# Optimization experiments

Measured on AMD Instinct MI355X. Metric: run time of the kernel, lower is better.

The kernel has to match this reference:

```python
import jax, jax.numpy as jnp
import numpy as np

E = 1024  # embed_dim
H = 16    # num_heads
D = E // H  # head_dim


def setup_inputs() -> dict:
    key = jax.random.key(0)
    ks = jax.random.split(key, 9)
    s = 0.02
    return {
        "hidden_state": jax.random.normal(ks[0], (4, 1024, E), jnp.float32),
        "Wq": jax.random.normal(ks[1], (H, D, E), jnp.float32) * s,
        "bq": jax.random.normal(ks[2], (H, D), jnp.float32) * s,
        "Wk": jax.random.normal(ks[3], (H, D, E), jnp.float32) * s,
        "bk": jax.random.normal(ks[4], (H, D), jnp.float32) * s,
        "Wv": jax.random.normal(ks[5], (H, D, E), jnp.float32) * s,
        "bv": jax.random.normal(ks[6], (H, D), jnp.float32) * s,
        "Wo": jax.random.normal(ks[7], (E, E), jnp.float32) * s,
        "bo": jax.random.normal(ks[8], (E,), jnp.float32) * s,
    }


def _mha(x, Wq, bq, Wk, bk, Wv, bv, Wo, bo):
    # Per-head linear projections (torch Linear: y = x W^T + b), batched over heads.
    q = jnp.einsum("bse,hde->bhsd", x, Wq) + bq[None, :, None, :]
    k = jnp.einsum("bse,hde->bhsd", x, Wk) + bk[None, :, None, :]
    v = jnp.einsum("bse,hde->bhsd", x, Wv) + bv[None, :, None, :]
    scores = jnp.einsum("bhsd,bhtd->bhst", q, k) / jnp.sqrt(jnp.asarray(D, x.dtype))
    w = jax.nn.softmax(scores, axis=-1)  # F.softmax default -> last dim
    o = jnp.einsum("bhst,bhtd->bhsd", w, v)
    # concat heads along last dim: [B,S,H*D] in head order (matches torch.cat)
    B, _, S, _ = o.shape
    o = jnp.transpose(o, (0, 2, 1, 3)).reshape(B, S, H * D)
    return o @ Wo.T + bo


def reference(hidden_state, Wq, bq, Wk, bk, Wv, bv, Wo, bo):
    return _mha(hidden_state, Wq, bq, Wk, bk, Wv, bv, Wo, bo)
```

## Files before the change

### kernel.cpp

```cpp
#include <hip/hip_runtime.h>
#include <hip/hip_bf16.h>
#include <stdint.h>

#define E_DIM 1024
#define H_NUM 16
#define D_DIM 64
#define B_NUM 4
#define S_LEN 1024

typedef __attribute__((ext_vector_type(8))) short bf16x8;
typedef __attribute__((ext_vector_type(4))) short bf16x4;
typedef __attribute__((ext_vector_type(4))) float f32x4;

#define SOFTMAX_C2 0.18033688011112042f

__device__ inline ushort f2b(float x) {
    __hip_bfloat16 h = __float2bfloat16(x);
    return *(ushort*)&h;
}
__device__ inline float b2f(ushort u) {
    __hip_bfloat16 h = *(__hip_bfloat16*)&u;
    return __bfloat162float(h);
}
__device__ inline uint pk2(float a, float b) {
    __hip_bfloat162 h = __float22bfloat162_rn(make_float2(a, b));
    return *(uint*)&h;
}
__device__ inline float fexp2(float x) { return __builtin_amdgcn_exp2f(x); }

__device__ inline uint pk2h(float a, float b) {
    uint ua = __builtin_bit_cast(uint, a) + 0x8000u;
    uint ub = __builtin_bit_cast(uint, b) + 0x8000u;
    return __builtin_amdgcn_perm(ub, ua, 0x07060302u);
}

__device__ inline void gld16(const ushort* g, ushort* l) {
    __builtin_amdgcn_global_load_lds((const __attribute__((address_space(1))) void*)g,
                                     (__attribute__((address_space(3))) void*)l, 16, 0, 0);
}

__global__ __launch_bounds__(256)
void convert_all(const float* __restrict__ X,  const float* __restrict__ Wq,
                 const float* __restrict__ Wk, const float* __restrict__ Wv,
                 const float* __restrict__ Wo,
                 ushort* __restrict__ Xb, ushort* __restrict__ Wcat,
                 ushort* __restrict__ Wob)
{
    const int bid = blockIdx.x;
    const float* src; ushort* dst; size_t off;
    if (bid < 4096)      { src = X;  dst = Xb;   off = (size_t)bid * 1024; }
    else if (bid < 5120) { src = Wq; dst = Wcat;              off = (size_t)(bid - 4096) * 1024; }
    else if (bid < 6144) { src = Wk; dst = Wcat + (1u << 20); off = (size_t)(bid - 5120) * 1024; }
    else if (bid < 7168) { src = Wv; dst = Wcat + (2u << 20); off = (size_t)(bid - 6144) * 1024; }
    else                 { src = Wo; dst = Wob;               off = (size_t)(bid - 7168) * 1024; }
    const size_t i = off + (size_t)threadIdx.x * 4;
    float4 v = *(const float4*)&src[i];
    ushort4 o;
    o.x = f2b(v.x); o.y = f2b(v.y); o.z = f2b(v.z); o.w = f2b(v.w);
    *(ushort4*)&dst[i] = o;
}

__global__ __launch_bounds__(256, 4)
void gemm_qkv(const ushort* __restrict__ A, const ushort* __restrict__ Bw,
              const float* __restrict__ b0, const float* __restrict__ b1,
              const float* __restrict__ b2,
              ushort* __restrict__ Qb, ushort* __restrict__ Kb,
              ushort* __restrict__ Vt_g, int K)
{
    __shared__ __align__(16) ushort SM[17408];
    ushort* As = SM;
    ushort* Bs = SM + 8192;

    const int tid  = threadIdx.x;
    const int wave = tid >> 6;
    const int lane = tid & 63;
    const int quad = lane >> 4;
    const int l16  = lane & 15;
    const int wm   = wave & 1;
    const int wn   = wave >> 1;

    const int bid = blockIdx.x;
    const int xcd = bid & 7;
    const int j   = bid >> 3;
    const int jm  = j / 24;
    const int jn  = j - jm * 24;
    const int m0  = (xcd * 4 + jm) * 128;
    const int n0  = jn * 128;

    f32x4 acc[4][4] = {};

    auto stageA = [&](int k0) {
#pragma unroll
        for (int i = 0; i < 4; ++i) {
            const int e   = i * 256 + tid;
            const int row = e >> 3;
            const int gc8 = ((e & 7) ^ (row & 7)) * 8;
            gld16(&A[(size_t)(m0 + row) * K + k0 + gc8], &As[e * 8]);
        }
    };
    auto stageB = [&](int k0) {
#pragma unroll
        for (int i = 0; i < 4; ++i) {
            const int e   = i * 256 + tid;
            const int row = e >> 3;
            const int gc8 = ((e & 7) ^ (row & 7)) * 8;
            gld16(&Bw[(size_t)(n0 + row) * K + k0 + gc8], &Bs[e * 8]);
        }
    };

    const int nk = K >> 6;
    const int xa = (l16 & 7) * 8;
    for (int ki = 0; ki < nk; ++ki) {
        stageA(ki << 6); stageB(ki << 6);
        __syncthreads();

#pragma unroll
        for (int ks = 0; ks < 2; ++ks) {
            const int lc = (ks * 32 + quad * 8) ^ xa;
            bf16x8 af[4], bf[4];
#pragma unroll
            for (int mi = 0; mi < 4; ++mi)
                af[mi] = *(const bf16x8*)&As[(wm * 64 + mi * 16 + l16) * 64 + lc];
#pragma unroll
            for (int ni = 0; ni < 4; ++ni)
                bf[ni] = *(const bf16x8*)&Bs[(wn * 64 + ni * 16 + l16) * 64 + lc];
#pragma unroll
            for (int mi = 0; mi < 4; ++mi)
#pragma unroll
                for (int ni = 0; ni < 4; ++ni)
                    acc[mi][ni] = __builtin_amdgcn_mfma_f32_16x16x32_bf16(af[mi], bf[ni], acc[mi][ni], 0, 0, 0);
        }
        __syncthreads();
    }

    const int seg   = n0 >> 10;
    const int cbase = n0 & 1023;
    const float* bp = (seg == 0) ? b0 : (seg == 1) ? b1 : b2;
    const float scl = (seg == 0) ? SOFTMAX_C2 : 1.0f;

    if (seg < 2) {
        ushort* T = SM;
#pragma unroll
        for (int ni = 0; ni < 4; ++ni) {
            const int nloc = wn * 64 + ni * 16 + l16;
            const float bv = bp[cbase + nloc];
#pragma unroll
            for (int mi = 0; mi < 4; ++mi)
#pragma unroll
                for (int r = 0; r < 4; ++r)
                    T[(wm * 64 + mi * 16 + quad * 4 + r) * 136 + nloc] =
                        f2b((acc[mi][ni][r] + bv) * scl);
        }
        __syncthreads();
        ushort* dst = (seg == 0) ? Qb : Kb;
        const int row = tid >> 1, half = tid & 1;
        const ushort* s = &T[row * 136 + half * 64];
        ushort* d = &dst[(size_t)(m0 + row) * 1024 + cbase + half * 64];
#pragma unroll
        for (int j2 = 0; j2 < 8; ++j2)
            *(uint4*)(d + j2 * 8) = *(const uint4*)(s + j2 * 8);
    } else {
        ushort* Tt = SM;
        const int b  = m0 >> 10, sbase = m0 & 1023;
#pragma unroll
        for (int ni = 0; ni < 4; ++ni) {
            const int nloc = wn * 64 + ni * 16 + l16;
            const float bv = bp[cbase + nloc];
#pragma unroll
            for (int mi = 0; mi < 4; ++mi) {
                const int mloc = wm * 64 + mi * 16 + quad * 4;
                ushort4 pk;
                pk.x = f2b(acc[mi][ni][0] + bv);
                pk.y = f2b(acc[mi][ni][1] + bv);
                pk.z = f2b(acc[mi][ni][2] + bv);
                pk.w = f2b(acc[mi][ni][3] + bv);
                *(ushort4*)&Tt[nloc * 136 + mloc] = pk;
            }
        }
        __syncthreads();
        const int nrow = tid >> 1, half = tid & 1;
        const int hh   = (cbase >> 6) + (nrow >> 6);
        const int drow = nrow & 63;
        const ushort* s = &Tt[nrow * 136 + half * 64];
        ushort* d = &Vt_g[(((size_t)(b * 16 + hh)) * 64 + drow) * 1024 + sbase + half * 64];
#pragma unroll
        for (int j2 = 0; j2 < 8; ++j2)
            *(uint4*)(d + j2 * 8) = *(const uint4*)(s + j2 * 8);
    }
}

__global__ __launch_bounds__(256, 4)
void attention16(const ushort* __restrict__ Qg, const ushort* __restrict__ Kg,
                 const ushort* __restrict__ Vg, ushort* __restrict__ Anorm)
{
    __shared__ __align__(16) ushort SM[16896];
    const int VOFF = 8192;

    const int tid  = threadIdx.x;
    const int w    = tid >> 6;
    const int lane = tid & 63;
    const int quad = lane >> 4;
    const int l16  = lane & 15;

    const int gid = blockIdx.x;
    const int qt  = (gid >> 3) & 15;
    const int bh  = (gid & 7) | ((gid >> 7) << 3);
    const int b   = bh >> 4;
    const int h   = bh & 15;
    const size_t tbase = ((size_t)b * S_LEN) * E_DIM + (size_t)h * D_DIM;
    const size_t vbase = (size_t)bh * D_DIM * S_LEN;

    const ushort* qrow = Qg + tbase + (size_t)(qt * 64 + w * 16 + l16) * E_DIM + quad * 8;
    bf16x8 qf[2];
    qf[0] = *(const bf16x8*)qrow;
    qf[1] = *(const bf16x8*)(qrow + 32);

    const int krow = tid >> 3, kslot = tid & 7;
    const int vr   = tid >> 2, vc = (tid & 3) * 8;

    const ushort* kptr = Kg + tbase + (size_t)krow * E_DIM + ((kslot ^ (krow & 7)) * 8);
    const ushort* vptr = Vg + vbase + (size_t)vr * S_LEN + vc;

    gld16(kptr,              &SM[tid * 8]);
    gld16(kptr + 32 * E_DIM, &SM[(256 + tid) * 8]);
    {
        uint4 v0 = *(const uint4*)vptr;
        uint4 v1 = *(const uint4*)(vptr + 32);
        *(uint4*)&SM[VOFF + vr * 68 + vc]      = v0;
        *(uint4*)&SM[VOFF + vr * 68 + vc + 32] = v1;
    }
    __syncthreads();

    float lq = 0.0f;
    f32x4 oacc[4] = {};
    const int xk = (l16 & 7);

    for (int kt = 0; kt < 16; ++kt) {
        const int cur = kt & 1;

        uint4 vpre0, vpre1;
        if (kt < 15) {
            kptr += 64 * E_DIM;
            gld16(kptr,              &SM[(cur ^ 1) * 4096 + tid * 8]);
            gld16(kptr + 32 * E_DIM, &SM[(cur ^ 1) * 4096 + (256 + tid) * 8]);
            vptr += 64;
            vpre0 = *(const uint4*)vptr;
            vpre1 = *(const uint4*)(vptr + 32);
        }

        f32x4 sacc[4] = {};
#pragma unroll
        for (int mt = 0; mt < 4; ++mt)
#pragma unroll
            for (int ks = 0; ks < 2; ++ks) {
                bf16x8 kf = *(const bf16x8*)&SM[cur * 4096 + (mt * 16 + l16) * 64 +
                                                (((ks * 4 + quad) ^ xk) * 8)];
                sacc[mt] = __builtin_amdgcn_mfma_f32_16x16x32_bf16(kf, qf[ks], sacc[mt], 0, 0, 0);
            }

        bf16x4 pf[4];
        float rs = 0.0f;
#pragma unroll
        for (int mt = 0; mt < 4; ++mt) {
            float p0 = fexp2(sacc[mt][0]);
            float p1 = fexp2(sacc[mt][1]);
            float p2 = fexp2(sacc[mt][2]);
            float p3 = fexp2(sacc[mt][3]);
            rs += (p0 + p1) + (p2 + p3);
            union { uint uu[2]; bf16x4 v; } pk;
            pk.uu[0] = pk2h(p0, p1);
            pk.uu[1] = pk2h(p2, p3);
            pf[mt] = pk.v;
        }
        lq += rs;

#pragma unroll
        for (int nb = 0; nb < 4; ++nb)
#pragma unroll
            for (int kb = 0; kb < 4; ++kb) {
                bf16x4 vf = *(const bf16x4*)&SM[VOFF + cur * 4352 +
                                                (nb * 16 + l16) * 68 + kb * 16 + quad * 4];
                oacc[nb] = __builtin_amdgcn_mfma_f32_16x16x16bf16_1k(pf[kb], vf, oacc[nb], 0, 0, 0);
            }

        if (kt < 15) {
            *(uint4*)&SM[VOFF + (cur ^ 1) * 4352 + vr * 68 + vc]      = vpre0;
            *(uint4*)&SM[VOFF + (cur ^ 1) * 4352 + vr * 68 + vc + 32] = vpre1;
        }
        __syncthreads();
    }

    lq += __shfl_xor(lq, 16);
    lq += __shfl_xor(lq, 32);

    float linv[4];
#pragma unroll
    for (int r = 0; r < 4; ++r)
        linv[r] = __builtin_amdgcn_rcpf(__shfl(lq, quad * 4 + r));

    ushort* T = SM;
#pragma unroll
    for (int nb = 0; nb < 4; ++nb)
#pragma unroll
        for (int r = 0; r < 4; ++r)
            T[(w * 16 + quad * 4 + r) * 72 + nb * 16 + l16] = f2b(oacc[nb][r] * linv[r]);
    __syncthreads();
    {
        const int row = tid >> 2, c16 = (tid & 3) * 16;
        const ushort* s = &T[row * 72 + c16];
        ushort* d = &Anorm[(size_t)(b * 1024 + qt * 64 + row) * 1024 + h * 64 + c16];
        *(uint4*)(d)     = *(const uint4*)(s);
        *(uint4*)(d + 8) = *(const uint4*)(s + 8);
    }
}

__global__ __launch_bounds__(256, 2)
void gemm_out(const ushort* __restrict__ A, const ushort* __restrict__ Bw,
              const float* __restrict__ bias, float* __restrict__ Cout)
{
    __shared__ __align__(16) ushort SM[24576];
    ushort* As = SM;
    ushort* Bs = SM + 16384;

    const int tid  = threadIdx.x;
    const int wave = tid >> 6;
    const int lane = tid & 63;
    const int quad = lane >> 4;
    const int l16  = lane & 15;
    const int wm   = wave & 1;
    const int wn   = wave >> 1;

    const int bid = blockIdx.x;
    const int xcd = bid & 7;
    const int j   = bid >> 3;
    const int m0  = (xcd * 4 + (j & 3)) * 128;
    const int n0  = (j >> 2) * 64;

    f32x4 acc[4][2] = {};

    auto stageA = [&](int buf, int k0) {
#pragma unroll
        for (int i = 0; i < 4; ++i) {
            const int e   = i * 256 + tid;
            const int row = e >> 3;
            const int gc8 = ((e & 7) ^ (row & 7)) * 8;
            gld16(&A[(size_t)(m0 + row) * 1024 + k0 + gc8], &As[buf * 8192 + e * 8]);
        }
    };
    auto stageB = [&](int buf, int k0) {
#pragma unroll
        for (int i = 0; i < 2; ++i) {
            const int e   = i * 256 + tid;
            const int row = e >> 3;
            const int gc8 = ((e & 7) ^ (row & 7)) * 8;
            gld16(&Bw[(size_t)(n0 + row) * 1024 + k0 + gc8], &Bs[buf * 4096 + e * 8]);
        }
    };

    stageA(0, 0); stageB(0, 0);
    __syncthreads();

    const int xa = (l16 & 7) * 8;
    for (int ki = 0; ki < 16; ++ki) {
        const int cur = ki & 1;
        if (ki + 1 < 16) { stageA(cur ^ 1, (ki + 1) << 6); stageB(cur ^ 1, (ki + 1) << 6); }

#pragma unroll
        for (int ks = 0; ks < 2; ++ks) {
            const int lc = (ks * 32 + quad * 8) ^ xa;
            bf16x8 af[4], bf[2];
#pragma unroll
            for (int mi = 0; mi < 4; ++mi)
                af[mi] = *(const bf16x8*)&As[cur * 8192 + (wm * 64 + mi * 16 + l16) * 64 + lc];
#pragma unroll
            for (int ni = 0; ni < 2; ++ni)
                bf[ni] = *(const bf16x8*)&Bs[cur * 4096 + (wn * 32 + ni * 16 + l16) * 64 + lc];
#pragma unroll
            for (int mi = 0; mi < 4; ++mi)
#pragma unroll
                for (int ni = 0; ni < 2; ++ni)
                    acc[mi][ni] = __builtin_amdgcn_mfma_f32_16x16x32_bf16(af[mi], bf[ni], acc[mi][ni], 0, 0, 0);
        }
        __syncthreads();
    }

    float* Tf = (float*)SM;
#pragma unroll
    for (int ni = 0; ni < 2; ++ni) {
        const int nloc = wn * 32 + ni * 16 + l16;
        const float bv = bias[n0 + nloc];
#pragma unroll
        for (int mi = 0; mi < 4; ++mi)
#pragma unroll
            for (int r = 0; r < 4; ++r)
                Tf[(wm * 64 + mi * 16 + quad * 4 + r) * 68 + nloc] = acc[mi][ni][r] + bv;
    }
    __syncthreads();
    {
        const int row = tid >> 1, half = tid & 1;
        const float* s = &Tf[row * 68 + half * 32];
        float* d = &Cout[(size_t)(m0 + row) * 1024 + n0 + half * 32];
#pragma unroll
        for (int j2 = 0; j2 < 8; ++j2)
            *(float4*)(d + j2 * 4) = *(const float4*)(s + j2 * 4);
    }
}

extern "C" void kernel_launch(void* const* d_in, const int* in_sizes, int n_in,
                              void* d_out, int out_size, void* d_ws, size_t ws_size,
                              hipStream_t stream)
{
    (void)in_sizes; (void)n_in; (void)out_size; (void)ws_size;

    const float* X  = (const float*)d_in[0];
    const float* Wq = (const float*)d_in[1];
    const float* bq = (const float*)d_in[2];
    const float* Wk = (const float*)d_in[3];
    const float* bk = (const float*)d_in[4];
    const float* Wv = (const float*)d_in[5];
    const float* bv = (const float*)d_in[6];
    const float* Wo = (const float*)d_in[7];
    const float* bo = (const float*)d_in[8];

    const size_t MEG = 1u << 20;
    ushort* ws    = (ushort*)d_ws;
    ushort* Xb    = ws;
    ushort* Wcat  = ws + 4 * MEG;
    ushort* Wob   = ws + 7 * MEG;
    ushort* Qb    = ws + 8 * MEG;
    ushort* Kb    = ws + 12 * MEG;
    ushort* Vtg   = ws + 16 * MEG;
    ushort* Anorm = ws + 20 * MEG;

    dim3 blk(256);

    convert_all<<<8192, blk, 0, stream>>>(X, Wq, Wk, Wv, Wo, Xb, Wcat, Wob);

    gemm_qkv<<<768, blk, 0, stream>>>(Xb, Wcat, bq, bk, bv,
                                      Qb, Kb, Vtg, E_DIM);

    attention16<<<1024, blk, 0, stream>>>(Qb, Kb, Vtg, Anorm);

    gemm_out<<<512, blk, 0, stream>>>(Anorm, Wob, bo, (float*)d_out);
}
```

Baseline: 169.0 us.

## Fuse fp32-to-bf16 conversion of X and QKV weights into QKV GEMM staging

Removes the separate conversion pass for X and Wq/Wk/Wv; the QKV GEMM now loads fp32 directly, packs to bf16 in registers and stores to LDS. Only Wo is still pre-converted. This removes a large read/write round trip through memory, but replaces asynchronous global-to-LDS loads with synchronous register loads and doubles the bytes each tile fetches, with occupancy hint lowered to 3.

```diff
diff --git a/kernel.cpp b/kernel.cpp
--- a/kernel.cpp
+++ b/kernel.cpp
@@ -18,14 +18,6 @@
     __hip_bfloat16 h = __float2bfloat16(x);
     return *(ushort*)&h;
 }
-__device__ inline float b2f(ushort u) {
-    __hip_bfloat16 h = *(__hip_bfloat16*)&u;
-    return __bfloat162float(h);
-}
-__device__ inline uint pk2(float a, float b) {
-    __hip_bfloat162 h = __float22bfloat162_rn(make_float2(a, b));
-    return *(uint*)&h;
-}
 __device__ inline float fexp2(float x) { return __builtin_amdgcn_exp2f(x); }
 
 __device__ inline uint pk2h(float a, float b) {
@@ -40,32 +32,22 @@
 }
 
 __global__ __launch_bounds__(256)
-void convert_all(const float* __restrict__ X,  const float* __restrict__ Wq,
-                 const float* __restrict__ Wk, const float* __restrict__ Wv,
-                 const float* __restrict__ Wo,
-                 ushort* __restrict__ Xb, ushort* __restrict__ Wcat,
-                 ushort* __restrict__ Wob)
+void convert_wo(const float* __restrict__ Wo, ushort* __restrict__ Wob)
 {
-    const int bid = blockIdx.x;
-    const float* src; ushort* dst; size_t off;
-    if (bid < 4096)      { src = X;  dst = Xb;   off = (size_t)bid * 1024; }
-    else if (bid < 5120) { src = Wq; dst = Wcat;              off = (size_t)(bid - 4096) * 1024; }
-    else if (bid < 6144) { src = Wk; dst = Wcat + (1u << 20); off = (size_t)(bid - 5120) * 1024; }
-    else if (bid < 7168) { src = Wv; dst = Wcat + (2u << 20); off = (size_t)(bid - 6144) * 1024; }
-    else                 { src = Wo; dst = Wob;               off = (size_t)(bid - 7168) * 1024; }
-    const size_t i = off + (size_t)threadIdx.x * 4;
-    float4 v = *(const float4*)&src[i];
+    const size_t i = (size_t)blockIdx.x * 1024 + threadIdx.x * 4;
+    float4 v = *(const float4*)&Wo[i];
     ushort4 o;
     o.x = f2b(v.x); o.y = f2b(v.y); o.z = f2b(v.z); o.w = f2b(v.w);
-    *(ushort4*)&dst[i] = o;
-}
-
-__global__ __launch_bounds__(256, 4)
-void gemm_qkv(const ushort* __restrict__ A, const ushort* __restrict__ Bw,
+    *(ushort4*)&Wob[i] = o;
+}
+
+__global__ __launch_bounds__(256, 3)
+void gemm_qkv(const float* __restrict__ X,  const float* __restrict__ Wq,
+              const float* __restrict__ Wk, const float* __restrict__ Wv,
               const float* __restrict__ b0, const float* __restrict__ b1,
               const float* __restrict__ b2,
               ushort* __restrict__ Qb, ushort* __restrict__ Kb,
-              ushort* __restrict__ Vt_g, int K)
+              ushort* __restrict__ Vt_g)
 {
     __shared__ __align__(16) ushort SM[17408];
     ushort* As = SM;
@@ -87,31 +69,34 @@
     const int m0  = (xcd * 4 + jm) * 128;
     const int n0  = jn * 128;
 
+    const int seg   = n0 >> 10;
+    const int cbase = n0 & 1023;
+    const float* bsrc = (seg == 0) ? Wq : (seg == 1) ? Wk : Wv;
+
     f32x4 acc[4][4] = {};
 
-    auto stageA = [&](int k0) {
+    auto stage = [&](const float* __restrict__ src, int rbase, ushort* dst, int k0) {
 #pragma unroll
         for (int i = 0; i < 4; ++i) {
             const int e   = i * 256 + tid;
             const int row = e >> 3;
             const int gc8 = ((e & 7) ^ (row & 7)) * 8;
-            gld16(&A[(size_t)(m0 + row) * K + k0 + gc8], &As[e * 8]);
+            const float* s = &src[(size_t)(rbase + row) * 1024 + k0 + gc8];
+            float4 f0 = *(const float4*)s;
+            float4 f1 = *(const float4*)(s + 4);
+            union { uint uu[4]; uint4 v; } pk;
+            pk.uu[0] = pk2h(f0.x, f0.y);
+            pk.uu[1] = pk2h(f0.z, f0.w);
+            pk.uu[2] = pk2h(f1.x, f1.y);
+            pk.uu[3] = pk2h(f1.z, f1.w);
+            *(uint4*)&dst[e * 8] = pk.v;
         }
     };
-    auto stageB = [&](int k0) {
-#pragma unroll
-        for (int i = 0; i < 4; ++i) {
-            const int e   = i * 256 + tid;
-            const int row = e >> 3;
-            const int gc8 = ((e & 7) ^ (row & 7)) * 8;
-            gld16(&Bw[(size_t)(n0 + row) * K + k0 + gc8], &Bs[e * 8]);
-        }
-    };
-
-    const int nk = K >> 6;
+
     const int xa = (l16 & 7) * 8;
-    for (int ki = 0; ki < nk; ++ki) {
-        stageA(ki << 6); stageB(ki << 6);
+    for (int ki = 0; ki < 16; ++ki) {
+        stage(X,    m0,    As, ki << 6);
+        stage(bsrc, cbase, Bs, ki << 6);
         __syncthreads();
 
 #pragma unroll
@@ -133,8 +118,6 @@
         __syncthreads();
     }
 
-    const int seg   = n0 >> 10;
-    const int cbase = n0 & 1023;
     const float* bp = (seg == 0) ? b0 : (seg == 1) ? b1 : b2;
     const float scl = (seg == 0) ? SOFTMAX_C2 : 1.0f;
 
@@ -424,20 +407,18 @@
 
     const size_t MEG = 1u << 20;
     ushort* ws    = (ushort*)d_ws;
-    ushort* Xb    = ws;
-    ushort* Wcat  = ws + 4 * MEG;
-    ushort* Wob   = ws + 7 * MEG;
-    ushort* Qb    = ws + 8 * MEG;
-    ushort* Kb    = ws + 12 * MEG;
-    ushort* Vtg   = ws + 16 * MEG;
-    ushort* Anorm = ws + 20 * MEG;
+    ushort* Wob   = ws;
+    ushort* Qb    = ws + 1 * MEG;
+    ushort* Kb    = ws + 5 * MEG;
+    ushort* Vtg   = ws + 9 * MEG;
+    ushort* Anorm = ws + 13 * MEG;
 
     dim3 blk(256);
 
-    convert_all<<<8192, blk, 0, stream>>>(X, Wq, Wk, Wv, Wo, Xb, Wcat, Wob);
-
-    gemm_qkv<<<768, blk, 0, stream>>>(Xb, Wcat, bq, bk, bv,
-                                      Qb, Kb, Vtg, E_DIM);
+    convert_wo<<<1024, blk, 0, stream>>>(Wo, Wob);
+
+    gemm_qkv<<<768, blk, 0, stream>>>(X, Wq, Wk, Wv, bq, bk, bv,
+                                      Qb, Kb, Vtg);
 
     attention16<<<1024, blk, 0, stream>>>(Qb, Kb, Vtg, Anorm);
 
```

Result: slower. 186.9 us (+10.6%).
